# Performance work log

Hardware: AMD Instinct MI355X
Metric: run time of the kernel (lower is better)

## Reference

```python
import jax, jax.numpy as jnp
import numpy as np

B, S, H = 1, 1024, 1024
E = 1024          # expert_dim
NEXP = 16         # num_experts
TOPK = 2
ALPHA = 1.702
LIMIT = 7.0


def setup_inputs() -> dict:
    key = jax.random.key(0)
    ks = jax.random.split(key, 8)
    hidden_states = jax.random.normal(ks[0], (B, S, H), dtype=jnp.float32)
    # router (gate): Linear(H, NEXP) with bias
    Wg = jax.random.normal(ks[1], (NEXP, H), dtype=jnp.float32) / np.sqrt(H)
    bg = jax.random.normal(ks[2], (NEXP,), dtype=jnp.float32) * 0.01
    # per-expert gate_up_proj: Linear(H, 2E) -> store as [NEXP, H, 2E]
    Wgu = jax.random.normal(ks[3], (NEXP, H, 2 * E), dtype=jnp.float32) / np.sqrt(H)
    bgu = jax.random.normal(ks[4], (NEXP, 2 * E), dtype=jnp.float32) * 0.01
    # per-expert down_proj: Linear(E, H) -> store as [NEXP, E, H]
    Wd = jax.random.normal(ks[5], (NEXP, E, H), dtype=jnp.float32) / np.sqrt(E)
    bd = jax.random.normal(ks[6], (NEXP, H), dtype=jnp.float32) * 0.01
    return {"hidden_states": hidden_states, "Wg": Wg, "bg": bg,
            "Wgu": Wgu, "bgu": bgu, "Wd": Wd, "bd": bd}


def _moe_forward(x, Wg, bg, Wgu, bgu, Wd, bd):
    b, s, h = x.shape
    xt = x.reshape(-1, h)                                   # [T, H]
    # router
    logits = xt @ Wg.T + bg                                 # [T, NEXP]
    # gpt_oss routing: topk over raw logits, softmax over selected
    top_vals, top_idx = jax.lax.top_k(logits, TOPK)         # [T, K]
    rw = jax.nn.softmax(top_vals.astype(jnp.float32), axis=-1).astype(xt.dtype)
    # combine weight per (token, expert): zero for unselected experts
    onehot = jax.nn.one_hot(top_idx, NEXP, dtype=xt.dtype)  # [T, K, NEXP]
    cw = jnp.einsum("tk,tke->te", rw, onehot)               # [T, NEXP]
    # dense expert compute (reference math identical to gather/scatter version)
    gu = jnp.einsum("th,ehf->tef", xt, Wgu) + bgu[None]     # [T, NEXP, 2E]
    gate = gu[..., ::2]
    up = gu[..., 1::2]
    gate = jnp.minimum(gate, LIMIT)
    up = jnp.clip(up, -LIMIT, LIMIT)
    glu = gate * jax.nn.sigmoid(gate * ALPHA)
    gated = (up + 1.0) * glu                                # [T, NEXP, E]
    out_e = jnp.einsum("tef,efh->teh", gated, Wd) + bd[None]  # [T, NEXP, H]
    out = jnp.einsum("teh,te->th", out_e, cw)               # [T, H]
    return out.reshape(b, s, h)


def reference(hidden_states, Wg, bg, Wgu, bgu, Wd, bd):
    return _moe_forward(hidden_states, Wg, bg, Wgu, bgu, Wd, bd)
```

## Files before the change

kernel.cpp:

```cpp
#include <hip/hip_runtime.h>
#include <hip/hip_bf16.h>

#define NT 1024
#define HD 1024
#define ED 1024
#define F2D 2048
#define NEXPERT 16
#define GROWS 2304
#define ALPHA_C 1.702f
#define LIMIT_C 7.0f

typedef float f32x4 __attribute__((ext_vector_type(4)));
typedef short short8 __attribute__((ext_vector_type(8)));
typedef unsigned int u32x4 __attribute__((ext_vector_type(4)));

__device__ __forceinline__ unsigned short f2bf(float x) {
  union { float f; unsigned int u; } v; v.f = x;
  unsigned int r = v.u + 0x7FFFu + ((v.u >> 16) & 1u);
  return (unsigned short)(r >> 16);
}
__device__ __forceinline__ unsigned int pk2(float lo, float hi) {
  return (unsigned int)f2bf(lo) | ((unsigned int)f2bf(hi) << 16);
}
__device__ __forceinline__ void async16(const void* g, void* l) {
  __builtin_amdgcn_global_load_lds((const __attribute__((address_space(1))) void*)g,
                                   (__attribute__((address_space(3))) void*)l, 16, 0, 0);
}

__global__ __launch_bounds__(64) void k_router(const float* __restrict__ x,
                                               const float* __restrict__ Wg,
                                               const float* __restrict__ bg,
                                               const float* __restrict__ bd,
                                               int* __restrict__ e01,
                                               float* __restrict__ w0f,
                                               float* __restrict__ w1f,
                                               unsigned short* __restrict__ Xbf,
                                               float* __restrict__ out) {
  const int t = blockIdx.x;
  const int l = threadIdx.x;
  const float4* x4 = (const float4*)(x + (size_t)t * HD);
  for (int i = 0; i < 4; ++i) {
    const int idx = l + 64 * i;
    float4 v = x4[idx];
    unsigned int a = pk2(v.x, v.y);
    unsigned int b = pk2(v.z, v.w);
    unsigned int* dst = (unsigned int*)(Xbf + (size_t)t * HD + idx * 4);
    dst[0] = a; dst[1] = b;
  }
  const int e = l & 15, qq = l >> 4;
  const float4* wg4 = (const float4*)(Wg + (size_t)e * HD);
  float s = 0.f;
  for (int j = 0; j < 64; ++j) {
    const int idx = qq + 4 * j;
    float4 a = x4[idx], b = wg4[idx];
    s += a.x * b.x + a.y * b.y + a.z * b.z + a.w * b.w;
  }
  s += __shfl_xor(s, 16);
  s += __shfl_xor(s, 32);
  const float logit = s + bg[e];
  float v0 = -1e30f, v1 = -1e30f; int i0 = 0, i1 = 0;
  for (int k = 0; k < 16; ++k) {
    float lv = __shfl(logit, k);
    if (lv > v0) { v1 = v0; i1 = i0; v0 = lv; i0 = k; }
    else if (lv > v1) { v1 = lv; i1 = k; }
  }
  const float w0 = 1.f / (1.f + __expf(v1 - v0));
  const float w1 = 1.f - w0;
  if (l == 0) {
    e01[t] = i0 | (i1 << 8);
    w0f[t] = w0;
    w1f[t] = w1;
  }
  const float4* bd0 = (const float4*)(bd + (size_t)i0 * HD);
  const float4* bd1 = (const float4*)(bd + (size_t)i1 * HD);
  float4* o4 = (float4*)(out + (size_t)t * HD);
  for (int i = 0; i < 4; ++i) {
    const int idx = l + 64 * i;
    float4 a = bd0[idx], b = bd1[idx];
    float4 r;
    r.x = w0 * a.x + w1 * b.x;
    r.y = w0 * a.y + w1 * b.y;
    r.z = w0 * a.z + w1 * b.z;
    r.w = w0 * a.w + w1 * b.w;
    o4[idx] = r;
  }
}

__global__ __launch_bounds__(1024) void k_scan(const int* __restrict__ e01,
                                               const float* __restrict__ w0f,
                                               const float* __restrict__ w1f,
                                               int* __restrict__ cnt,
                                               int* __restrict__ off,
                                               int* __restrict__ gtok,
                                               float* __restrict__ gwt) {
  __shared__ int scnt[NEXPERT];
  __shared__ int soff[NEXPERT];
  __shared__ int scur[NEXPERT];
  const int t = threadIdx.x;
  if (t < NEXPERT) { scnt[t] = 0; scur[t] = 0; }
  __syncthreads();
  const int p = e01[t];
  const int e0 = p & 255, e1 = p >> 8;
  atomicAdd(&scnt[e0], 1);
  atomicAdd(&scnt[e1], 1);
  __syncthreads();
  if (t == 0) {
    int a = 0;
    for (int e = 0; e < NEXPERT; ++e) { soff[e] = a; off[e] = a; cnt[e] = scnt[e]; a += scnt[e]; }
  }
  __syncthreads();
  int s0 = atomicAdd(&scur[e0], 1);
  int g0 = soff[e0] + s0;
  gtok[g0] = t; gwt[g0] = w0f[t];
  int s1 = atomicAdd(&scur[e1], 1);
  int g1 = soff[e1] + s1;
  gtok[g1] = t; gwt[g1] = w1f[t];
}

__global__ __launch_bounds__(256, 4) void k_gemm1(const unsigned short* __restrict__ Xbf,
                                                  const float* __restrict__ Wgu,
                                                  const float* __restrict__ bgu,
                                                  const int* __restrict__ cnt,
                                                  const int* __restrict__ off,
                                                  const int* __restrict__ gtok,
                                                  unsigned short* __restrict__ Gact) {
  const int e = blockIdx.z;
  const int Ne = cnt[e];
  const int mtile = blockIdx.y;
  if (mtile * 128 >= Ne) return;
  const int ntile = blockIdx.x;
  const int tid = threadIdx.x;
  const int lane = tid & 63;
  const int w = tid >> 6;
  const int wm = w & 1, wn = w >> 1;
  const int q = lane >> 4;
  const int fr = lane & 15;

  __shared__ unsigned short Alds[2 * 128 * 32];
  __shared__ unsigned int Blds[2 * 16 * 68];

  const int base = off[e] + mtile * 128;
  const int r0 = w * 32 + (lane >> 2);
  const int r1 = r0 + 16;
  const int c4a = lane & 3;
  const int gs0 = base + (((mtile * 128 + r0) < Ne) ? r0 : 0);
  const int gs1 = base + (((mtile * 128 + r1) < Ne) ? r1 : 0);
  const unsigned short* gp0 = Xbf + (size_t)gtok[gs0] * HD + c4a * 8;
  const unsigned short* gp1 = Xbf + (size_t)gtok[gs1] * HD + c4a * 8;
  const int lofs = w * 1024;

  const int k2 = tid >> 4;
  const int c4 = tid & 15;
  const float* Wb = Wgu + (size_t)e * HD * F2D + (size_t)(2 * k2) * F2D + ntile * 64 + c4 * 4;

  f32x4 acc[4][2] = {};
  float4 ba, bb;

  ba = *(const float4*)Wb;
  bb = *(const float4*)(Wb + F2D);
  async16(gp0, Alds + lofs);
  async16(gp1, Alds + lofs + 512);
  {
    u32x4 pkv;
    pkv[0] = pk2(ba.x, bb.x); pkv[1] = pk2(ba.y, bb.y);
    pkv[2] = pk2(ba.z, bb.z); pkv[3] = pk2(ba.w, bb.w);
    *(u32x4*)(Blds + k2 * 68 + c4 * 4) = pkv;
  }
  __syncthreads();

#pragma unroll 2
  for (int ks = 0; ks < 32; ++ks) {
    const int cur = ks & 1, nxt = cur ^ 1;
    const bool more = (ks + 1) < 32;
    if (more) {
      const float* bp = Wb + (size_t)(ks + 1) * 32 * F2D;
      ba = *(const float4*)bp;
      bb = *(const float4*)(bp + F2D);
      async16(gp0 + (ks + 1) * 32, Alds + nxt * 4096 + lofs);
      async16(gp1 + (ks + 1) * 32, Alds + nxt * 4096 + lofs + 512);
    }
    short8 af[4], bfr[2];
#pragma unroll
    for (int mi = 0; mi < 4; ++mi)
      af[mi] = *(const short8*)(Alds + cur * 4096 + (wm * 64 + mi * 16 + fr) * 32 + q * 8);
#pragma unroll
    for (int ni = 0; ni < 2; ++ni) {
      const unsigned int* p = Blds + cur * 1088 + q * 4 * 68 + wn * 32 + ni * 16 + fr;
      union { unsigned int u[4]; short8 s; } uu;
      uu.u[0] = p[0]; uu.u[1] = p[68]; uu.u[2] = p[136]; uu.u[3] = p[204];
      bfr[ni] = uu.s;
    }
#pragma unroll
    for (int mi = 0; mi < 4; ++mi)
#pragma unroll
      for (int ni = 0; ni < 2; ++ni)
        acc[mi][ni] = __builtin_amdgcn_mfma_f32_16x16x32_bf16(af[mi], bfr[ni], acc[mi][ni], 0, 0, 0);
    if (more) {
      u32x4 pkv;
      pkv[0] = pk2(ba.x, bb.x); pkv[1] = pk2(ba.y, bb.y);
      pkv[2] = pk2(ba.z, bb.z); pkv[3] = pk2(ba.w, bb.w);
      *(u32x4*)(Blds + nxt * 1088 + k2 * 68 + c4 * 4) = pkv;
    }
    __syncthreads();
  }

  const float* bguE = bgu + (size_t)e * F2D + ntile * 64;
#pragma unroll
  for (int mi = 0; mi < 4; ++mi) {
    const int rowb = wm * 64 + mi * 16 + q * 4;
#pragma unroll
    for (int ni = 0; ni < 2; ++ni) {
      const int col = wn * 32 + ni * 16 + fr;
      const float bias = bguE[col];
#pragma unroll
      for (int r = 0; r < 4; ++r) {
        float v = acc[mi][ni][r] + bias;
        float pv = __shfl_xor(v, 1);
        float gate = (lane & 1) ? pv : v;
        float up   = (lane & 1) ? v : pv;
        gate = fminf(gate, LIMIT_C);
        up = fminf(fmaxf(up, -LIMIT_C), LIMIT_C);
        float glu = gate / (1.f + __expf(-ALPHA_C * gate));
        float val = (up + 1.f) * glu;
        const int s = rowb + r;
        if (!(lane & 1) && (mtile * 128 + s) < Ne)
          Gact[(size_t)(base + s) * ED + ntile * 32 + (col >> 1)] = f2bf(val);
      }
    }
  }
}

__global__ __launch_bounds__(256, 4) void k_gemm2(const unsigned short* __restrict__ Gact,
                                                  const float* __restrict__ Wd,
                                                  const int* __restrict__ cnt,
                                                  const int* __restrict__ off,
                                                  const int* __restrict__ gtok,
                                                  const float* __restrict__ gwt,
                                                  float* __restrict__ out) {
  const int z = blockIdx.z;
  const int e = z >> 1, ksp = z & 1;
  const int Ne = cnt[e];
  const int mtile = blockIdx.y;
  if (mtile * 128 >= Ne) return;
  const int ntile = blockIdx.x;
  const int tid = threadIdx.x;
  const int lane = tid & 63;
  const int w = tid >> 6;
  const int wm = w & 1, wn = w >> 1;
  const int q = lane >> 4;
  const int fr = lane & 15;

  __shared__ unsigned short Alds[2 * 128 * 32];
  __shared__ unsigned int Blds[2 * 16 * 68];

  const int base = off[e] + mtile * 128;
  const int r0 = w * 32 + (lane >> 2);
  const int r1 = r0 + 16;
  const int c4a = lane & 3;
  const unsigned short* gp0 = Gact + (size_t)(base + r0) * ED + ksp * 512 + c4a * 8;
  const unsigned short* gp1 = Gact + (size_t)(base + r1) * ED + ksp * 512 + c4a * 8;
  const int lofs = w * 1024;

  const int k2 = tid >> 4;
  const int c4 = tid & 15;
  const float* Wb = Wd + (size_t)e * ED * HD + (size_t)(ksp * 512 + 2 * k2) * HD + ntile * 64 + c4 * 4;

  f32x4 acc[4][2] = {};
  float4 ba, bb;

  ba = *(const float4*)Wb;
  bb = *(const float4*)(Wb + HD);
  async16(gp0, Alds + lofs);
  async16(gp1, Alds + lofs + 512);
  {
    u32x4 pkv;
    pkv[0] = pk2(ba.x, bb.x); pkv[1] = pk2(ba.y, bb.y);
    pkv[2] = pk2(ba.z, bb.z); pkv[3] = pk2(ba.w, bb.w);
    *(u32x4*)(Blds + k2 * 68 + c4 * 4) = pkv;
  }
  __syncthreads();

#pragma unroll 2
  for (int ks = 0; ks < 16; ++ks) {
    const int cur = ks & 1, nxt = cur ^ 1;
    const bool more = (ks + 1) < 16;
    if (more) {
      const float* bp = Wb + (size_t)(ks + 1) * 32 * HD;
      ba = *(const float4*)bp;
      bb = *(const float4*)(bp + HD);
      async16(gp0 + (ks + 1) * 32, Alds + nxt * 4096 + lofs);
      async16(gp1 + (ks + 1) * 32, Alds + nxt * 4096 + lofs + 512);
    }
    short8 af[4], bfr[2];
#pragma unroll
    for (int mi = 0; mi < 4; ++mi)
      af[mi] = *(const short8*)(Alds + cur * 4096 + (wm * 64 + mi * 16 + fr) * 32 + q * 8);
#pragma unroll
    for (int ni = 0; ni < 2; ++ni) {
      const unsigned int* p = Blds + cur * 1088 + q * 4 * 68 + wn * 32 + ni * 16 + fr;
      union { unsigned int u[4]; short8 s; } uu;
      uu.u[0] = p[0]; uu.u[1] = p[68]; uu.u[2] = p[136]; uu.u[3] = p[204];
      bfr[ni] = uu.s;
    }
#pragma unroll
    for (int mi = 0; mi < 4; ++mi)
#pragma unroll
      for (int ni = 0; ni < 2; ++ni)
        acc[mi][ni] = __builtin_amdgcn_mfma_f32_16x16x32_bf16(af[mi], bfr[ni], acc[mi][ni], 0, 0, 0);
    if (more) {
      u32x4 pkv;
      pkv[0] = pk2(ba.x, bb.x); pkv[1] = pk2(ba.y, bb.y);
      pkv[2] = pk2(ba.z, bb.z); pkv[3] = pk2(ba.w, bb.w);
      *(u32x4*)(Blds + nxt * 1088 + k2 * 68 + c4 * 4) = pkv;
    }
    __syncthreads();
  }

#pragma unroll
  for (int mi = 0; mi < 4; ++mi) {
    const int rowb = wm * 64 + mi * 16 + q * 4;
#pragma unroll
    for (int r = 0; r < 4; ++r) {
      const int s = rowb + r;
      if ((mtile * 128 + s) < Ne) {
        const int gsl = base + s;
        const int tok = gtok[gsl];
        const float wt = gwt[gsl];
        float* op = out + (size_t)tok * HD + ntile * 64;
#pragma unroll
        for (int ni = 0; ni < 2; ++ni) {
          const int col = wn * 32 + ni * 16 + fr;
          atomicAdd(op + col, wt * acc[mi][ni][r]);
        }
      }
    }
  }
}

extern "C" void kernel_launch(void* const* d_in, const int* in_sizes, int n_in,
                              void* d_out, int out_size, void* d_ws, size_t ws_size,
                              hipStream_t stream) {
  const float* x   = (const float*)d_in[0];
  const float* Wg  = (const float*)d_in[1];
  const float* bg  = (const float*)d_in[2];
  const float* Wgu = (const float*)d_in[3];
  const float* bgu = (const float*)d_in[4];
  const float* Wd  = (const float*)d_in[5];
  const float* bd  = (const float*)d_in[6];
  float* out = (float*)d_out;

  int* cnt = (int*)d_ws;
  int* off = cnt + 16;
  int* e01 = off + 16;
  float* w0f = (float*)(e01 + NT);
  float* w1f = w0f + NT;
  int* gtok = (int*)(w1f + NT);
  float* gwt = (float*)(gtok + GROWS);
  unsigned short* Xbf = (unsigned short*)(gwt + GROWS);
  unsigned short* Gact = Xbf + (size_t)NT * HD;

  k_router<<<NT, 64, 0, stream>>>(x, Wg, bg, bd, e01, w0f, w1f, Xbf, out);
  k_scan<<<1, NT, 0, stream>>>(e01, w0f, w1f, cnt, off, gtok, gwt);
  k_gemm1<<<dim3(32, 8, NEXPERT), 256, 0, stream>>>(Xbf, Wgu, bgu, cnt, off, gtok, Gact);
  k_gemm2<<<dim3(16, 8, 2 * NEXPERT), 256, 0, stream>>>(Gact, Wd, cnt, off, gtok, gwt, out);
}
```

Baseline: 345.9 us.

## Replace LDS-staged GEMMs with register-direct fragment loads and smaller M tiles

Both expert GEMMs drop LDS staging and block-wide barriers. Each wave now loads its A and B MFMA fragments straight from global memory into registers, double-buffered two K-steps ahead. The M tile shrinks from 128 to 64 rows, which doubles grid.y, and the split-K in the down projection is removed. This cuts LDS traffic and synchronisation, but the waves no longer share loads: each fp32 weight element is read strided, a column per lane across rows, which risks uncoalesced global accesses and more redundant traffic.

```diff
diff --git a/kernel.cpp b/kernel.cpp
--- a/kernel.cpp
+++ b/kernel.cpp
@@ -12,7 +12,6 @@
 
 typedef float f32x4 __attribute__((ext_vector_type(4)));
 typedef short short8 __attribute__((ext_vector_type(8)));
-typedef unsigned int u32x4 __attribute__((ext_vector_type(4)));
 
 __device__ __forceinline__ unsigned short f2bf(float x) {
   union { float f; unsigned int u; } v; v.f = x;
@@ -21,10 +20,6 @@
 }
 __device__ __forceinline__ unsigned int pk2(float lo, float hi) {
   return (unsigned int)f2bf(lo) | ((unsigned int)f2bf(hi) << 16);
-}
-__device__ __forceinline__ void async16(const void* g, void* l) {
-  __builtin_amdgcn_global_load_lds((const __attribute__((address_space(1))) void*)g,
-                                   (__attribute__((address_space(3))) void*)l, 16, 0, 0);
 }
 
 __global__ __launch_bounds__(64) void k_router(const float* __restrict__ x,
@@ -110,11 +105,9 @@
   }
   __syncthreads();
   int s0 = atomicAdd(&scur[e0], 1);
-  int g0 = soff[e0] + s0;
-  gtok[g0] = t; gwt[g0] = w0f[t];
+  gtok[soff[e0] + s0] = t; gwt[soff[e0] + s0] = w0f[t];
   int s1 = atomicAdd(&scur[e1], 1);
-  int g1 = soff[e1] + s1;
-  gtok[g1] = t; gwt[g1] = w1f[t];
+  gtok[soff[e1] + s1] = t; gwt[soff[e1] + s1] = w1f[t];
 }
 
 __global__ __launch_bounds__(256, 4) void k_gemm1(const unsigned short* __restrict__ Xbf,
@@ -127,105 +120,76 @@
   const int e = blockIdx.z;
   const int Ne = cnt[e];
   const int mtile = blockIdx.y;
-  if (mtile * 128 >= Ne) return;
+  if (mtile * 64 >= Ne) return;
   const int ntile = blockIdx.x;
   const int tid = threadIdx.x;
   const int lane = tid & 63;
-  const int w = tid >> 6;
-  const int wm = w & 1, wn = w >> 1;
+  const int wv = tid >> 6;
   const int q = lane >> 4;
   const int fr = lane & 15;
-
-  __shared__ unsigned short Alds[2 * 128 * 32];
-  __shared__ unsigned int Blds[2 * 16 * 68];
-
-  const int base = off[e] + mtile * 128;
-  const int r0 = w * 32 + (lane >> 2);
-  const int r1 = r0 + 16;
-  const int c4a = lane & 3;
-  const int gs0 = base + (((mtile * 128 + r0) < Ne) ? r0 : 0);
-  const int gs1 = base + (((mtile * 128 + r1) < Ne) ? r1 : 0);
-  const unsigned short* gp0 = Xbf + (size_t)gtok[gs0] * HD + c4a * 8;
-  const unsigned short* gp1 = Xbf + (size_t)gtok[gs1] * HD + c4a * 8;
-  const int lofs = w * 1024;
-
-  const int k2 = tid >> 4;
-  const int c4 = tid & 15;
-  const float* Wb = Wgu + (size_t)e * HD * F2D + (size_t)(2 * k2) * F2D + ntile * 64 + c4 * 4;
-
-  f32x4 acc[4][2] = {};
-  float4 ba, bb;
-
-  ba = *(const float4*)Wb;
-  bb = *(const float4*)(Wb + F2D);
-  async16(gp0, Alds + lofs);
-  async16(gp1, Alds + lofs + 512);
-  {
-    u32x4 pkv;
-    pkv[0] = pk2(ba.x, bb.x); pkv[1] = pk2(ba.y, bb.y);
-    pkv[2] = pk2(ba.z, bb.z); pkv[3] = pk2(ba.w, bb.w);
-    *(u32x4*)(Blds + k2 * 68 + c4 * 4) = pkv;
-  }
-  __syncthreads();
+  const int base = off[e] + mtile * 64;
+
+  const unsigned short* ap[4];
+#pragma unroll
+  for (int mi = 0; mi < 4; ++mi) {
+    const int rloc = mi * 16 + fr;
+    const int gs = base + ((mtile * 64 + rloc < Ne) ? rloc : 0);
+    ap[mi] = Xbf + (size_t)gtok[gs] * HD + q * 8;
+  }
+  const int col = ntile * 64 + wv * 16 + fr;
+  const float* bp = Wgu + (size_t)e * HD * F2D + (size_t)(q * 8) * F2D + col;
+
+  short8 areg[2][4];
+  float breg[2][8];
+  f32x4 acc[4] = {};
+
+#pragma unroll
+  for (int s = 0; s < 2; ++s) {
+#pragma unroll
+    for (int mi = 0; mi < 4; ++mi) areg[s][mi] = *(const short8*)(ap[mi] + s * 32);
+    const float* b = bp + (size_t)s * 32 * F2D;
+#pragma unroll
+    for (int j = 0; j < 8; ++j) breg[s][j] = b[(size_t)j * F2D];
+  }
 
 #pragma unroll 2
   for (int ks = 0; ks < 32; ++ks) {
-    const int cur = ks & 1, nxt = cur ^ 1;
-    const bool more = (ks + 1) < 32;
-    if (more) {
-      const float* bp = Wb + (size_t)(ks + 1) * 32 * F2D;
-      ba = *(const float4*)bp;
-      bb = *(const float4*)(bp + F2D);
-      async16(gp0 + (ks + 1) * 32, Alds + nxt * 4096 + lofs);
-      async16(gp1 + (ks + 1) * 32, Alds + nxt * 4096 + lofs + 512);
-    }
-    short8 af[4], bfr[2];
+    const int s = ks & 1;
+    union { unsigned int u[4]; short8 s8; } uu;
+    uu.u[0] = pk2(breg[s][0], breg[s][1]);
+    uu.u[1] = pk2(breg[s][2], breg[s][3]);
+    uu.u[2] = pk2(breg[s][4], breg[s][5]);
+    uu.u[3] = pk2(breg[s][6], breg[s][7]);
+    const short8 bfrag = uu.s8;
 #pragma unroll
     for (int mi = 0; mi < 4; ++mi)
-      af[mi] = *(const short8*)(Alds + cur * 4096 + (wm * 64 + mi * 16 + fr) * 32 + q * 8);
-#pragma unroll
-    for (int ni = 0; ni < 2; ++ni) {
-      const unsigned int* p = Blds + cur * 1088 + q * 4 * 68 + wn * 32 + ni * 16 + fr;
-      union { unsigned int u[4]; short8 s; } uu;
-      uu.u[0] = p[0]; uu.u[1] = p[68]; uu.u[2] = p[136]; uu.u[3] = p[204];
-      bfr[ni] = uu.s;
-    }
-#pragma unroll
-    for (int mi = 0; mi < 4; ++mi)
-#pragma unroll
-      for (int ni = 0; ni < 2; ++ni)
-        acc[mi][ni] = __builtin_amdgcn_mfma_f32_16x16x32_bf16(af[mi], bfr[ni], acc[mi][ni], 0, 0, 0);
-    if (more) {
-      u32x4 pkv;
-      pkv[0] = pk2(ba.x, bb.x); pkv[1] = pk2(ba.y, bb.y);
-      pkv[2] = pk2(ba.z, bb.z); pkv[3] = pk2(ba.w, bb.w);
-      *(u32x4*)(Blds + nxt * 1088 + k2 * 68 + c4 * 4) = pkv;
-    }
-    __syncthreads();
-  }
-
-  const float* bguE = bgu + (size_t)e * F2D + ntile * 64;
+      acc[mi] = __builtin_amdgcn_mfma_f32_16x16x32_bf16(areg[s][mi], bfrag, acc[mi], 0, 0, 0);
+    if (ks < 30) {
+      const int kn = ks + 2;
+#pragma unroll
+      for (int mi = 0; mi < 4; ++mi) areg[s][mi] = *(const short8*)(ap[mi] + kn * 32);
+      const float* b = bp + (size_t)kn * 32 * F2D;
+#pragma unroll
+      for (int j = 0; j < 8; ++j) breg[s][j] = b[(size_t)j * F2D];
+    }
+  }
+
+  const float bias = bgu[(size_t)e * F2D + col];
 #pragma unroll
   for (int mi = 0; mi < 4; ++mi) {
-    const int rowb = wm * 64 + mi * 16 + q * 4;
-#pragma unroll
-    for (int ni = 0; ni < 2; ++ni) {
-      const int col = wn * 32 + ni * 16 + fr;
-      const float bias = bguE[col];
-#pragma unroll
-      for (int r = 0; r < 4; ++r) {
-        float v = acc[mi][ni][r] + bias;
-        float pv = __shfl_xor(v, 1);
-        float gate = (lane & 1) ? pv : v;
-        float up   = (lane & 1) ? v : pv;
-        gate = fminf(gate, LIMIT_C);
-        up = fminf(fmaxf(up, -LIMIT_C), LIMIT_C);
-        float glu = gate / (1.f + __expf(-ALPHA_C * gate));
-        float val = (up + 1.f) * glu;
-        const int s = rowb + r;
-        if (!(lane & 1) && (mtile * 128 + s) < Ne)
-          Gact[(size_t)(base + s) * ED + ntile * 32 + (col >> 1)] = f2bf(val);
-      }
+#pragma unroll
+    for (int r = 0; r < 4; ++r) {
+      const int srow = mi * 16 + q * 4 + r;
+      float v = acc[mi][r] + bias;
+      float pv = __shfl_xor(v, 1);
+      float gate = (lane & 1) ? pv : v;
+      float up   = (lane & 1) ? v : pv;
+      gate = fminf(gate, LIMIT_C);
+      up = fminf(fmaxf(up, -LIMIT_C), LIMIT_C);
+      float glu = gate / (1.f + __expf(-ALPHA_C * gate));
+      float val = (up + 1.f) * glu;
+      if (!(lane & 1) && (mtile * 64 + srow) < Ne)
+        Gact[(size_t)(base + srow) * ED + (col >> 1)] = f2bf(val);
     }
   }
 }
@@ -237,101 +201,70 @@
                                                   const int* __restrict__ gtok,
                                                   const float* __restrict__ gwt,
                                                   float* __restrict__ out) {
-  const int z = blockIdx.z;
-  const int e = z >> 1, ksp = z & 1;
+  const int e = blockIdx.z;
   const int Ne = cnt[e];
   const int mtile = blockIdx.y;
-  if (mtile * 128 >= Ne) return;
+  if (mtile * 64 >= Ne) return;
   const int ntile = blockIdx.x;
   const int tid = threadIdx.x;
   const int lane = tid & 63;
-  const int w = tid >> 6;
-  const int wm = w & 1, wn = w >> 1;
+  const int wv = tid >> 6;
   const int q = lane >> 4;
   const int fr = lane & 15;
-
-  __shared__ unsigned short Alds[2 * 128 * 32];
-  __shared__ unsigned int Blds[2 * 16 * 68];
-
-  const int base = off[e] + mtile * 128;
-  const int r0 = w * 32 + (lane >> 2);
-  const int r1 = r0 + 16;
-  const int c4a = lane & 3;
-  const unsigned short* gp0 = Gact + (size_t)(base + r0) * ED + ksp * 512 + c4a * 8;
-  const unsigned short* gp1 = Gact + (size_t)(base + r1) * ED + ksp * 512 + c4a * 8;
-  const int lofs = w * 1024;
-
-  const int k2 = tid >> 4;
-  const int c4 = tid & 15;
-  const float* Wb = Wd + (size_t)e * ED * HD + (size_t)(ksp * 512 + 2 * k2) * HD + ntile * 64 + c4 * 4;
-
-  f32x4 acc[4][2] = {};
-  float4 ba, bb;
-
-  ba = *(const float4*)Wb;
-  bb = *(const float4*)(Wb + HD);
-  async16(gp0, Alds + lofs);
-  async16(gp1, Alds + lofs + 512);
-  {
-    u32x4 pkv;
-    pkv[0] = pk2(ba.x, bb.x); pkv[1] = pk2(ba.y, bb.y);
-    pkv[2] = pk2(ba.z, bb.z); pkv[3] = pk2(ba.w, bb.w);
-    *(u32x4*)(Blds + k2 * 68 + c4 * 4) = pkv;
-  }
-  __syncthreads();
+  const int base = off[e] + mtile * 64;
+
+  const unsigned short* ap[4];
+#pragma unroll
+  for (int mi = 0; mi < 4; ++mi)
+    ap[mi] = Gact + (size_t)(base + mi * 16 + fr) * ED + q * 8;
+  const int col = ntile * 64 + wv * 16 + fr;
+  const float* bp = Wd + (size_t)e * ED * HD + (size_t)(q * 8) * HD + col;
+
+  short8 areg[2][4];
+  float breg[2][8];
+  f32x4 acc[4] = {};
+
+#pragma unroll
+  for (int s = 0; s < 2; ++s) {
+#pragma unroll
+    for (int mi = 0; mi < 4; ++mi) areg[s][mi] = *(const short8*)(ap[mi] + s * 32);
+    const float* b = bp + (size_t)s * 32 * HD;
+#pragma unroll
+    for (int j = 0; j < 8; ++j) breg[s][j] = b[(size_t)j * HD];
+  }
 
 #pragma unroll 2
-  for (int ks = 0; ks < 16; ++ks) {
-    const int cur = ks & 1, nxt = cur ^ 1;
-    const bool more = (ks + 1) < 16;
-    if (more) {
-      const float* bp = Wb + (size_t)(ks + 1) * 32 * HD;
-      ba = *(const float4*)bp;
-      bb = *(const float4*)(bp + HD);
-      async16(gp0 + (ks + 1) * 32, Alds + nxt * 4096 + lofs);
-      async16(gp1 + (ks + 1) * 32, Alds + nxt * 4096 + lofs + 512);
-    }
-    short8 af[4], bfr[2];
+  for (int ks = 0; ks < 32; ++ks) {
+    const int s = ks & 1;
+    union { unsigned int u[4]; short8 s8; } uu;
+    uu.u[0] = pk2(breg[s][0], breg[s][1]);
+    uu.u[1] = pk2(breg[s][2], breg[s][3]);
+    uu.u[2] = pk2(breg[s][4], breg[s][5]);
+    uu.u[3] = pk2(breg[s][6], breg[s][7]);
+    const short8 bfrag = uu.s8;
 #pragma unroll
     for (int mi = 0; mi < 4; ++mi)
-      af[mi] = *(const short8*)(Alds + cur * 4096 + (wm * 64 + mi * 16 + fr) * 32 + q * 8);
-#pragma unroll
-    for (int ni = 0; ni < 2; ++ni) {
-      const unsigned int* p = Blds + cur * 1088 + q * 4 * 68 + wn * 32 + ni * 16 + fr;
-      union { unsigned int u[4]; short8 s; } uu;
-      uu.u[0] = p[0]; uu.u[1] = p[68]; uu.u[2] = p[136]; uu.u[3] = p[204];
-      bfr[ni] = uu.s;
-    }
-#pragma unroll
-    for (int mi = 0; mi < 4; ++mi)
-#pragma unroll
-      for (int ni = 0; ni < 2; ++ni)
-        acc[mi][ni] = __builtin_amdgcn_mfma_f32_16x16x32_bf16(af[mi], bfr[ni], acc[mi][ni], 0, 0, 0);
-    if (more) {
-      u32x4 pkv;
-      pkv[0] = pk2(ba.x, bb.x); pkv[1] = pk2(ba.y, bb.y);
-      pkv[2] = pk2(ba.z, bb.z); pkv[3] = pk2(ba.w, bb.w);
-      *(u32x4*)(Blds + nxt * 1088 + k2 * 68 + c4 * 4) = pkv;
-    }
-    __syncthreads();
+      acc[mi] = __builtin_amdgcn_mfma_f32_16x16x32_bf16(areg[s][mi], bfrag, acc[mi], 0, 0, 0);
+    if (ks < 30) {
+      const int kn = ks + 2;
+#pragma unroll
+      for (int mi = 0; mi < 4; ++mi) areg[s][mi] = *(const short8*)(ap[mi] + kn * 32);
+      const float* b = bp + (size_t)kn * 32 * HD;
+#pragma unroll
+      for (int j = 0; j < 8; ++j) breg[s][j] = b[(size_t)j * HD];
+    }
   }
 
 #pragma unroll
   for (int mi = 0; mi < 4; ++mi) {
-    const int rowb = wm * 64 + mi * 16 + q * 4;
 #pragma unroll
     for (int r = 0; r < 4; ++r) {
-      const int s = rowb + r;
-      if ((mtile * 128 + s) < Ne) {
-        const int gsl = base + s;
+      const int srow = mi * 16 + q * 4 + r;
+      if ((mtile * 64 + srow) < Ne) {
+        const int gsl = base + srow;
         const int tok = gtok[gsl];
         const float wt = gwt[gsl];
-        float* op = out + (size_t)tok * HD + ntile * 64;
-#pragma unroll
-        for (int ni = 0; ni < 2; ++ni) {
-          const int col = wn * 32 + ni * 16 + fr;
-          atomicAdd(op + col, wt * acc[mi][ni][r]);
-        }
+        atomicAdd(out + (size_t)tok * HD + col, wt * acc[mi][r]);
       }
     }
   }
@@ -361,6 +294,6 @@
 
   k_router<<<NT, 64, 0, stream>>>(x, Wg, bg, bd, e01, w0f, w1f, Xbf, out);
   k_scan<<<1, NT, 0, stream>>>(e01, w0f, w1f, cnt, off, gtok, gwt);
-  k_gemm1<<<dim3(32, 8, NEXPERT), 256, 0, stream>>>(Xbf, Wgu, bgu, cnt, off, gtok, Gact);
-  k_gemm2<<<dim3(16, 8, 2 * NEXPERT), 256, 0, stream>>>(Gact, Wd, cnt, off, gtok, gwt, out);
-}
+  k_gemm1<<<dim3(32, 16, NEXPERT), 256, 0, stream>>>(Xbf, Wgu, bgu, cnt, off, gtok, Gact);
+  k_gemm2<<<dim3(16, 16, NEXPERT), 256, 0, stream>>>(Gact, Wd, cnt, off, gtok, gwt, out);
+}
```

New measurement: 405.8 us. 1.17x slower.
